# Kernel optimization log

Hardware: AMD Instinct MI355X
Metric: run time of the kernel (lower is better)

## Reference

```python
import jax, jax.numpy as jnp
import numpy as np

# Irreps layout: 128x0e + 64x1o + 32x2e  (mul, 2l+1)
MULS = [128, 64, 32]
DEGS = [1, 3, 5]
D = sum(m * d for m, d in zip(MULS, DEGS))  # 480
N = 200_000
G = 1000


def _split(x):
    """[N, D] -> list of [N, mul, deg] irrep blocks."""
    out, o = [], 0
    for m, d in zip(MULS, DEGS):
        out.append(x[:, o:o + m * d].reshape(-1, m, d))
        o += m * d
    return out


def _merge(blocks):
    return jnp.concatenate([b.reshape(b.shape[0], -1) for b in blocks], axis=-1)


def _equiv_linear(xb, Ws):
    """e3nn-style per-irrep channel-mixing linear with 1/sqrt(fan_in) norm."""
    return [jnp.einsum('nmd,mo->nod', x, W) / np.float32(np.sqrt(m))
            for x, W, m in zip(xb, Ws, MULS)]


def setup_inputs() -> dict:
    key = jax.random.key(0)
    ks = jax.random.split(key, 16)
    inp = {"f": jax.random.normal(ks[0], (N, D), jnp.float32)}
    i = 1
    for name in ["Wq", "Wk", "Wv", "Wd"]:
        for j, m in enumerate(MULS):
            inp[f"{name}{j}"] = jax.random.normal(ks[i], (m, m), jnp.float32)
            i += 1
    inp["batch"] = jnp.sort(jax.random.randint(ks[15], (N,), 0, G))
    inp["n_graphs"] = G
    return inp


def reference(f, Wq0, Wq1, Wq2, Wk0, Wk1, Wk2, Wv0, Wv1, Wv2,
              Wd0, Wd1, Wd2, batch, n_graphs):
    fb = _split(f)
    qb = _equiv_linear(fb, [Wq0, Wq1, Wq2])
    kb = _equiv_linear(fb, [Wk0, Wk1, Wk2])
    vb = _equiv_linear(fb, [Wv0, Wv1, Wv2])

    # FullyConnectedTensorProduct(q, k, '0e'): only paths with matching l
    # contribute; each path is a weighted channel-pair dot over m components.
    logits = jnp.zeros(f.shape[0], f.dtype)
    for q, k, W, m, d in zip(qb, kb, [Wd0, Wd1, Wd2], MULS, DEGS):
        logits = logits + jnp.einsum('nid,njd,ij->n', q, k, W) / np.float32(np.sqrt(m * m * d))
    logits = logits / np.float32(np.sqrt(len(MULS)))  # path-count normalization
    logits = logits * np.float32(1.0 / np.sqrt(D))    # self.scale buffer

    w = jnp.exp(logits)                                       # [N]
    norm = jax.ops.segment_sum(w, batch, num_segments=n_graphs)
    norm = jnp.clip(norm, 1e-8)
    v = _merge(vb)                                            # [N, D]
    num = jax.ops.segment_sum(v * w[:, None], batch, num_segments=n_graphs)
    return num / norm[:, None]                                # [G, D]
```

## Files before the change

kernel.cpp:

```cpp
#include <hip/hip_runtime.h>
#include <math.h>

#define D_TOT 480

typedef short bf16x8 __attribute__((ext_vector_type(8)));
typedef float f32x4 __attribute__((ext_vector_type(4)));

#define MFMA16(a, b, c) __builtin_amdgcn_mfma_f32_16x16x32_bf16((a), (b), (c), 0, 0, 0)

static __device__ __forceinline__ unsigned short f2bf(float x) {
  unsigned u = __float_as_uint(x);
  u += 0x7FFFu + ((u >> 16) & 1u);
  return (unsigned short)(u >> 16);
}

template <int M, int DEG, int BASE>
static __device__ void precompute_impl(
    const float* __restrict__ Wq, const float* __restrict__ Wk,
    const float* __restrict__ Wd, const float* __restrict__ Wv,
    unsigned short* __restrict__ Bp, int kt, float* lds) {
  float* sWkT = lds;
  float* sT   = lds + M * (M + 1);

  constexpr int TPR = 256 / M;
  constexpr int RPT = 32 / TPR;
  constexpr int nct = M / 8;
  constexpr int ktn = M / 32;

  int t = threadIdx.x;
  float scale = 1.0f / ((float)M * (float)M * sqrtf(1440.0f * (float)DEG));
  float sm = rsqrtf((float)M);

  for (int i = t; i < M * M; i += 256) {
    int r = i / M, c = i - r * M;
    sWkT[c * (M + 1) + r] = Wk[i];
  }

  {
    int c = t % M, r0 = t / M;
    float acc[RPT];
#pragma unroll
    for (int rr = 0; rr < RPT; ++rr) acc[rr] = 0.f;
#pragma unroll 4
    for (int a = 0; a < M; ++a) {
      float wd = Wd[a * M + c];
#pragma unroll
      for (int rr = 0; rr < RPT; ++rr)
        acc[rr] += Wq[(kt * 32 + r0 + rr * TPR) * M + a] * wd;
    }
    __syncthreads();
#pragma unroll
    for (int rr = 0; rr < RPT; ++rr) sT[(r0 + rr * TPR) * M + c] = acc[rr];
  }
  __syncthreads();

  {
    int j = t % M, r0 = t / M;
    float acc[RPT];
#pragma unroll
    for (int rr = 0; rr < RPT; ++rr) acc[rr] = 0.f;
#pragma unroll 4
    for (int c = 0; c < M; ++c) {
      float wk = sWkT[c * (M + 1) + j];
#pragma unroll
      for (int rr = 0; rr < RPT; ++rr)
        acc[rr] += sT[(r0 + rr * TPR) * M + c] * wk;
    }
    __syncthreads();
#pragma unroll
    for (int rr = 0; rr < RPT; ++rr) sT[(r0 + rr * TPR) * M + j] = acc[rr] * scale;
  }
  __syncthreads();

  for (int idx = t; idx < nct * 512; idx += 256) {
    int ct = idx >> 9, rem = idx & 511, l = rem >> 3, j = rem & 7;
    int kl = (l >> 4) * 8 + j;
    int c = ct * 16 + (l & 15);
    float val = (c < M) ? sT[kl * M + c] : Wv[(kt * 32 + kl) * M + (c - M)] * sm;
    Bp[BASE + (ct * ktn + kt) * 512 + rem] = f2bf(val);
  }
}

__global__ __launch_bounds__(256) void precompute_all(
    const float* __restrict__ Wq0, const float* __restrict__ Wq1, const float* __restrict__ Wq2,
    const float* __restrict__ Wk0, const float* __restrict__ Wk1, const float* __restrict__ Wk2,
    const float* __restrict__ Wd0, const float* __restrict__ Wd1, const float* __restrict__ Wd2,
    const float* __restrict__ Wv0, const float* __restrict__ Wv1, const float* __restrict__ Wv2,
    unsigned short* __restrict__ Bp) {
  extern __shared__ float lds[];
  int b = blockIdx.x;
  if (b < 4)      precompute_impl<128, 1, 0>(Wq0, Wk0, Wd0, Wv0, Bp, b, lds);
  else if (b < 6) precompute_impl<64, 3, 32768>(Wq1, Wk1, Wd1, Wv1, Bp, b - 4, lds);
  else            precompute_impl<32, 5, 40960>(Wq2, Wk2, Wd2, Wv2, Bp, 0, lds);
}

__global__ __launch_bounds__(256, 2) void fused_stat_kernel(
    const float* __restrict__ f, const unsigned short* __restrict__ Bpack,
    const int* __restrict__ batch,
    float* __restrict__ outnum, float* __restrict__ norm,
    int N, int tpb, int ntiles) {
  __shared__ float lds_logit[3][16];
  int t = threadIdx.x, w = t >> 6, lane = t & 63;
  int q = lane >> 4, lm = lane & 15;

  if (t < 48) ((float*)lds_logit)[t] = 0.f;
  __syncthreads();

  int t0 = blockIdx.x * tpb;
  int t1 = min(t0 + tpb, ntiles);
  if (t0 >= t1) return;

  const bf16x8* B0f = (const bf16x8*)Bpack;
  const bf16x8* B1f = (const bf16x8*)(Bpack + 32768);
  const bf16x8* B2f = (const bf16x8*)(Bpack + 40960);

  bf16x8 Bu0[2][4], Bv0[2][4], Bu1[2], Bv1[2], Bu2, Bv2;
#pragma unroll
  for (int ctl = 0; ctl < 2; ++ctl)
#pragma unroll
    for (int k = 0; k < 4; ++k) {
      Bu0[ctl][k] = B0f[((2 * w + ctl) * 4 + k) * 64 + lane];
      Bv0[ctl][k] = B0f[((2 * w + ctl + 8) * 4 + k) * 64 + lane];
    }
#pragma unroll
  for (int k = 0; k < 2; ++k) {
    Bu1[k] = B1f[(w * 2 + k) * 64 + lane];
    Bv1[k] = B1f[((w + 4) * 2 + k) * 64 + lane];
  }
  bool has2 = (w >= 2);
  int ct2 = has2 ? (w - 2) : 0;
  Bu2 = B2f[ct2 * 64 + lane];
  Bv2 = B2f[(ct2 + 2) * 64 + lane];

  float racc0[2] = {0.f, 0.f};
  float racc1[3] = {0.f, 0.f, 0.f};
  float racc2[5] = {0.f, 0.f, 0.f, 0.f, 0.f};
  float naccw = 0.f;
  int cur_g = -1;

  auto wavered = [&](float s) -> float {
    s += __shfl_xor(s, 16);
    s += __shfl_xor(s, 32);
    return s;
  };
  auto flushf = [&](int g) {
    float* og = outnum + (size_t)g * 480;
#pragma unroll
    for (int ctl = 0; ctl < 2; ++ctl) {
      float s = wavered(racc0[ctl]);
      if (lane < 16) atomicAdd(og + (2 * w + ctl) * 16 + lane, s);
      racc0[ctl] = 0.f;
    }
#pragma unroll
    for (int d = 0; d < 3; ++d) {
      float s = wavered(racc1[d]);
      if (lane < 16) atomicAdd(og + 128 + 3 * (w * 16 + lane) + d, s);
      racc1[d] = 0.f;
    }
    if (has2) {
#pragma unroll
      for (int d = 0; d < 5; ++d) {
        float s = wavered(racc2[d]);
        if (lane < 16) atomicAdd(og + 320 + 5 * (ct2 * 16 + lane) + d, s);
        racc2[d] = 0.f;
      }
    }
    if (w == 0) {
      float s = wavered(naccw);
      if (lane == 0) atomicAdd(norm + g, s);
      naccw = 0.f;
    }
  };

  for (int ti = t0; ti < t1; ++ti) {
    int p = ti % 3;
    int nt = ti * 16;
    int valid = min(16, N - nt);

    long rr = nt + (lm < valid ? lm : valid - 1);
    const float4* fr4 = reinterpret_cast<const float4*>(f + rr * 480);
    bf16x8 a0[4], a1[3][2], a2[5];
#pragma unroll
    for (int ks = 0; ks < 4; ++ks) {
      float4 A = fr4[ks * 8 + 2 * q];
      float4 B = fr4[ks * 8 + 2 * q + 1];
      bf16x8 v;
      v[0] = (short)f2bf(A.x); v[1] = (short)f2bf(A.y);
      v[2] = (short)f2bf(A.z); v[3] = (short)f2bf(A.w);
      v[4] = (short)f2bf(B.x); v[5] = (short)f2bf(B.y);
      v[6] = (short)f2bf(B.z); v[7] = (short)f2bf(B.w);
      a0[ks] = v;
    }
#pragma unroll
    for (int h = 0; h < 2; ++h) {
      unsigned short bb[24];
#pragma unroll
      for (int i = 0; i < 6; ++i) {
        float4 x4 = fr4[32 + 24 * h + 6 * q + i];
        bb[i * 4 + 0] = f2bf(x4.x); bb[i * 4 + 1] = f2bf(x4.y);
        bb[i * 4 + 2] = f2bf(x4.z); bb[i * 4 + 3] = f2bf(x4.w);
      }
#pragma unroll
      for (int d = 0; d < 3; ++d) {
        bf16x8 v;
#pragma unroll
        for (int j = 0; j < 8; ++j) v[j] = (short)bb[3 * j + d];
        a1[d][h] = v;
      }
    }
    {
      unsigned short bb[40];
#pragma unroll
      for (int i = 0; i < 10; ++i) {
        float4 x4 = fr4[80 + 10 * q + i];
        bb[i * 4 + 0] = f2bf(x4.x); bb[i * 4 + 1] = f2bf(x4.y);
        bb[i * 4 + 2] = f2bf(x4.z); bb[i * 4 + 3] = f2bf(x4.w);
      }
#pragma unroll
      for (int d = 0; d < 5; ++d) {
        bf16x8 v;
#pragma unroll
        for (int j = 0; j < 8; ++j) v[j] = (short)bb[5 * j + d];
        a2[d] = v;
      }
    }

    auto xg = [&](int r, int c) -> float {
      int nn = nt + q * 4 + r;
      if (nn >= N) nn = N - 1;
      return f[(size_t)nn * 480 + c];
    };

    float pl[4] = {0.f, 0.f, 0.f, 0.f};
#pragma unroll
    for (int ctl = 0; ctl < 2; ++ctl) {
      f32x4 u = {0.f, 0.f, 0.f, 0.f};
      u = MFMA16(a0[0], Bu0[ctl][0], u);
      u = MFMA16(a0[1], Bu0[ctl][1], u);
      u = MFMA16(a0[2], Bu0[ctl][2], u);
      u = MFMA16(a0[3], Bu0[ctl][3], u);
      int c = (2 * w + ctl) * 16 + lm;
#pragma unroll
      for (int r = 0; r < 4; ++r) pl[r] += u[r] * xg(r, c);
    }
#pragma unroll
    for (int d = 0; d < 3; ++d) {
      f32x4 u = {0.f, 0.f, 0.f, 0.f};
      u = MFMA16(a1[d][0], Bu1[0], u);
      u = MFMA16(a1[d][1], Bu1[1], u);
      int c = 128 + 3 * (w * 16 + lm) + d;
#pragma unroll
      for (int r = 0; r < 4; ++r) pl[r] += u[r] * xg(r, c);
    }
    if (has2) {
#pragma unroll
      for (int d = 0; d < 5; ++d) {
        f32x4 u = {0.f, 0.f, 0.f, 0.f};
        u = MFMA16(a2[d], Bu2, u);
        int c = 320 + 5 * (ct2 * 16 + lm) + d;
#pragma unroll
        for (int r = 0; r < 4; ++r) pl[r] += u[r] * xg(r, c);
      }
    }
#pragma unroll
    for (int off = 1; off < 16; off <<= 1) {
#pragma unroll
      for (int r = 0; r < 4; ++r) pl[r] += __shfl_xor(pl[r], off);
    }
    if (lm == 0) {
#pragma unroll
      for (int r = 0; r < 4; ++r) atomicAdd(&lds_logit[p][q * 4 + r], pl[r]);
    }
    __syncthreads();

    float wgt[4];
#pragma unroll
    for (int r = 0; r < 4; ++r) {
      int node = q * 4 + r;
      wgt[r] = (node < valid) ? __expf(lds_logit[p][node]) : 0.f;
    }
    if (t < 16) lds_logit[(ti + 2) % 3][t] = 0.f;

    {
      int nn = nt + (lm < valid ? lm : valid - 1);
      if (nn >= N) nn = N - 1;
      int gl = batch[nn];
      int gp = __shfl(gl, (lane == 0) ? 0 : lane - 1);
      unsigned long long bm = __ballot(lm > 0 && lm < valid && gl != gp);
      unsigned segm = (unsigned)bm & 0xFFFEu;

      int a = 0;
      while (a < valid) {
        unsigned hi = segm & ~((1u << (a + 1)) - 1u);
        int b = hi ? (int)__builtin_ctz(hi) : valid;
        int gs = __shfl(gl, a);
        if (gs != cur_g) {
          if (cur_g >= 0) flushf(cur_g);
          cur_g = gs;
        }
        int nq = q * 4;
        float m0 = (nq + 0 >= a && nq + 0 < b) ? wgt[0] : 0.f;
        float m1 = (nq + 1 >= a && nq + 1 < b) ? wgt[1] : 0.f;
        float m2 = (nq + 2 >= a && nq + 2 < b) ? wgt[2] : 0.f;
        float m3 = (nq + 3 >= a && nq + 3 < b) ? wgt[3] : 0.f;
        if (w == 0 && lm == 0) naccw += m0 + m1 + m2 + m3;
#pragma unroll
        for (int ctl = 0; ctl < 2; ++ctl) {
          f32x4 v = {0.f, 0.f, 0.f, 0.f};
          v = MFMA16(a0[0], Bv0[ctl][0], v);
          v = MFMA16(a0[1], Bv0[ctl][1], v);
          v = MFMA16(a0[2], Bv0[ctl][2], v);
          v = MFMA16(a0[3], Bv0[ctl][3], v);
          racc0[ctl] += m0 * v[0] + m1 * v[1] + m2 * v[2] + m3 * v[3];
        }
#pragma unroll
        for (int d = 0; d < 3; ++d) {
          f32x4 v = {0.f, 0.f, 0.f, 0.f};
          v = MFMA16(a1[d][0], Bv1[0], v);
          v = MFMA16(a1[d][1], Bv1[1], v);
          racc1[d] += m0 * v[0] + m1 * v[1] + m2 * v[2] + m3 * v[3];
        }
        if (has2) {
#pragma unroll
          for (int d = 0; d < 5; ++d) {
            f32x4 v = {0.f, 0.f, 0.f, 0.f};
            v = MFMA16(a2[d], Bv2, v);
            racc2[d] += m0 * v[0] + m1 * v[1] + m2 * v[2] + m3 * v[3];
          }
        }
        a = b;
      }
    }
  }
  if (cur_g >= 0) flushf(cur_g);
}

__global__ __launch_bounds__(256) void finalize_kernel(
    float* __restrict__ out, const float* __restrict__ norm, int total) {
  int idx = blockIdx.x * blockDim.x + threadIdx.x;
  if (idx < total) {
    int g = idx / 480;
    out[idx] = out[idx] / fmaxf(norm[g], 1e-8f);
  }
}

extern "C" void kernel_launch(void* const* d_in, const int* in_sizes, int n_in,
                              void* d_out, int out_size, void* d_ws, size_t ws_size,
                              hipStream_t stream) {
  const float* f   = (const float*)d_in[0];
  const int* batch = (const int*)d_in[13];

  int N = in_sizes[0] / D_TOT;
  int G = out_size / D_TOT;

  unsigned short* Bpack = (unsigned short*)d_ws;
  float* norm = (float*)((char*)d_ws + 86016);
  float* out  = (float*)d_out;

  hipMemsetAsync(d_out, 0, (size_t)out_size * sizeof(float), stream);
  hipMemsetAsync(norm, 0, (size_t)G * sizeof(float), stream);

  int lds128 = (128 * 129 + 32 * 128) * 4;
  hipFuncSetAttribute((const void*)precompute_all,
                      hipFuncAttributeMaxDynamicSharedMemorySize, lds128);
  precompute_all<<<7, 256, lds128, stream>>>(
      (const float*)d_in[1], (const float*)d_in[2], (const float*)d_in[3],
      (const float*)d_in[4], (const float*)d_in[5], (const float*)d_in[6],
      (const float*)d_in[10], (const float*)d_in[11], (const float*)d_in[12],
      (const float*)d_in[7], (const float*)d_in[8], (const float*)d_in[9],
      Bpack);

  int ntiles = (N + 15) / 16;
  int nblocks = 1024;
  if (nblocks > ntiles) nblocks = ntiles;
  int tpb = (ntiles + nblocks - 1) / nblocks;

  fused_stat_kernel<<<nblocks, 256, 0, stream>>>(
      f, Bpack, batch, out, norm, N, tpb, ntiles);

  finalize_kernel<<<(G * D_TOT + 255) / 256, 256, 0, stream>>>(out, norm, G * D_TOT);
}
```

Baseline: 309.7 us.

## Double-buffer input tiles in LDS via async global_load_lds with XOR swizzle

Each 16-row input tile is now staged into a double-buffered, XOR-swizzled LDS buffer with asynchronous global-to-LDS loads, and the next tile is prefetched while the current one is computed. All A-operand packing and the per-element gathers for the logits now read from LDS rather than global memory. The grid is halved to 512 blocks, which gives each block more tiles to pipeline. This uses about 60 KB of LDS per block, which can limit occupancy. It also relies on correct barrier placement, since the initial barrier was removed and there is no explicit wait on the async loads.

```diff
diff --git a/kernel.cpp b/kernel.cpp
--- a/kernel.cpp
+++ b/kernel.cpp
@@ -35,7 +35,6 @@
     int r = i / M, c = i - r * M;
     sWkT[c * (M + 1) + r] = Wk[i];
   }
-
   {
     int c = t % M, r0 = t / M;
     float acc[RPT];
@@ -53,7 +52,6 @@
     for (int rr = 0; rr < RPT; ++rr) sT[(r0 + rr * TPR) * M + c] = acc[rr];
   }
   __syncthreads();
-
   {
     int j = t % M, r0 = t / M;
     float acc[RPT];
@@ -71,7 +69,6 @@
     for (int rr = 0; rr < RPT; ++rr) sT[(r0 + rr * TPR) * M + j] = acc[rr] * scale;
   }
   __syncthreads();
-
   for (int idx = t; idx < nct * 512; idx += 256) {
     int ct = idx >> 9, rem = idx & 511, l = rem >> 3, j = rem & 7;
     int kl = (l >> 4) * 8 + j;
@@ -99,12 +96,12 @@
     const int* __restrict__ batch,
     float* __restrict__ outnum, float* __restrict__ norm,
     int N, int tpb, int ntiles) {
+  __shared__ __align__(16) char xsmem[2 * 30720];
   __shared__ float lds_logit[3][16];
   int t = threadIdx.x, w = t >> 6, lane = t & 63;
   int q = lane >> 4, lm = lane & 15;
 
   if (t < 48) ((float*)lds_logit)[t] = 0.f;
-  __syncthreads();
 
   int t0 = blockIdx.x * tpb;
   int t1 = min(t0 + tpb, ntiles);
@@ -131,6 +128,26 @@
   int ct2 = has2 ? (w - 2) : 0;
   Bu2 = B2f[ct2 * 64 + lane];
   Bv2 = B2f[(ct2 + 2) * 64 + lane];
+
+  auto stage = [&](int buf, int ti2) {
+    int nt2 = ti2 * 16;
+    int vmax = min(16, N - nt2) - 1;
+    char* dstbase = xsmem + buf * 30720;
+#pragma unroll
+    for (int k = 0; k < 8; ++k) {
+      int i = w + 4 * k;
+      if (i >= 30) break;
+      int D = i * 64 + lane;
+      int r = D / 120;
+      int g = (D - r * 120) ^ (r & 7);
+      int rc = r < vmax ? r : vmax;
+      const float* src = f + (size_t)(nt2 + rc) * 480 + g * 4;
+      __builtin_amdgcn_global_load_lds(
+          (const __attribute__((address_space(1))) void*)src,
+          (__attribute__((address_space(3))) void*)(dstbase + i * 1024),
+          16, 0, 0);
+    }
+  };
 
   float racc0[2] = {0.f, 0.f};
   float racc1[3] = {0.f, 0.f, 0.f};
@@ -172,18 +189,31 @@
     }
   };
 
-  for (int ti = t0; ti < t1; ++ti) {
+  stage(0, t0);
+
+  int cur = 0;
+  for (int ti = t0; ti < t1; ++ti, cur ^= 1) {
     int p = ti % 3;
     int nt = ti * 16;
     int valid = min(16, N - nt);
 
-    long rr = nt + (lm < valid ? lm : valid - 1);
-    const float4* fr4 = reinterpret_cast<const float4*>(f + rr * 480);
+    __syncthreads();
+    if (ti + 1 < t1) stage(cur ^ 1, ti + 1);
+
+    const char* xcur = xsmem + cur * 30720;
+    auto ld4 = [&](int r, int gr) -> float4 {
+      return *reinterpret_cast<const float4*>(xcur + r * 1920 + ((gr ^ (r & 7)) << 4));
+    };
+    auto ldf = [&](int r, int c) -> float {
+      return *reinterpret_cast<const float*>(
+          xcur + r * 1920 + ((((c >> 2)) ^ (r & 7)) << 4) + ((c & 3) << 2));
+    };
+
     bf16x8 a0[4], a1[3][2], a2[5];
 #pragma unroll
     for (int ks = 0; ks < 4; ++ks) {
-      float4 A = fr4[ks * 8 + 2 * q];
-      float4 B = fr4[ks * 8 + 2 * q + 1];
+      float4 A = ld4(lm, ks * 8 + 2 * q);
+      float4 B = ld4(lm, ks * 8 + 2 * q + 1);
       bf16x8 v;
       v[0] = (short)f2bf(A.x); v[1] = (short)f2bf(A.y);
       v[2] = (short)f2bf(A.z); v[3] = (short)f2bf(A.w);
@@ -192,44 +222,23 @@
       a0[ks] = v;
     }
 #pragma unroll
-    for (int h = 0; h < 2; ++h) {
-      unsigned short bb[24];
-#pragma unroll
-      for (int i = 0; i < 6; ++i) {
-        float4 x4 = fr4[32 + 24 * h + 6 * q + i];
-        bb[i * 4 + 0] = f2bf(x4.x); bb[i * 4 + 1] = f2bf(x4.y);
-        bb[i * 4 + 2] = f2bf(x4.z); bb[i * 4 + 3] = f2bf(x4.w);
-      }
-#pragma unroll
-      for (int d = 0; d < 3; ++d) {
+    for (int d = 0; d < 3; ++d)
+#pragma unroll
+      for (int h = 0; h < 2; ++h) {
         bf16x8 v;
 #pragma unroll
-        for (int j = 0; j < 8; ++j) v[j] = (short)bb[3 * j + d];
+        for (int j = 0; j < 8; ++j)
+          v[j] = (short)f2bf(ldf(lm, 128 + 3 * (h * 32 + q * 8 + j) + d));
         a1[d][h] = v;
       }
-    }
-    {
-      unsigned short bb[40];
-#pragma unroll
-      for (int i = 0; i < 10; ++i) {
-        float4 x4 = fr4[80 + 10 * q + i];
-        bb[i * 4 + 0] = f2bf(x4.x); bb[i * 4 + 1] = f2bf(x4.y);
-        bb[i * 4 + 2] = f2bf(x4.z); bb[i * 4 + 3] = f2bf(x4.w);
-      }
-#pragma unroll
-      for (int d = 0; d < 5; ++d) {
-        bf16x8 v;
-#pragma unroll
-        for (int j = 0; j < 8; ++j) v[j] = (short)bb[5 * j + d];
-        a2[d] = v;
-      }
-    }
-
-    auto xg = [&](int r, int c) -> float {
-      int nn = nt + q * 4 + r;
-      if (nn >= N) nn = N - 1;
-      return f[(size_t)nn * 480 + c];
-    };
+#pragma unroll
+    for (int d = 0; d < 5; ++d) {
+      bf16x8 v;
+#pragma unroll
+      for (int j = 0; j < 8; ++j)
+        v[j] = (short)f2bf(ldf(lm, 320 + 5 * (q * 8 + j) + d));
+      a2[d] = v;
+    }
 
     float pl[4] = {0.f, 0.f, 0.f, 0.f};
 #pragma unroll
@@ -241,7 +250,7 @@
       u = MFMA16(a0[3], Bu0[ctl][3], u);
       int c = (2 * w + ctl) * 16 + lm;
 #pragma unroll
-      for (int r = 0; r < 4; ++r) pl[r] += u[r] * xg(r, c);
+      for (int r = 0; r < 4; ++r) pl[r] += u[r] * ldf(q * 4 + r, c);
     }
 #pragma unroll
     for (int d = 0; d < 3; ++d) {
@@ -250,7 +259,7 @@
       u = MFMA16(a1[d][1], Bu1[1], u);
       int c = 128 + 3 * (w * 16 + lm) + d;
 #pragma unroll
-      for (int r = 0; r < 4; ++r) pl[r] += u[r] * xg(r, c);
+      for (int r = 0; r < 4; ++r) pl[r] += u[r] * ldf(q * 4 + r, c);
     }
     if (has2) {
 #pragma unroll
@@ -259,7 +268,7 @@
         u = MFMA16(a2[d], Bu2, u);
         int c = 320 + 5 * (ct2 * 16 + lm) + d;
 #pragma unroll
-        for (int r = 0; r < 4; ++r) pl[r] += u[r] * xg(r, c);
+        for (int r = 0; r < 4; ++r) pl[r] += u[r] * ldf(q * 4 + r, c);
       }
     }
 #pragma unroll
@@ -371,7 +380,7 @@
       Bpack);
 
   int ntiles = (N + 15) / 16;
-  int nblocks = 1024;
+  int nblocks = 512;
   if (nblocks > ntiles) nblocks = ntiles;
   int tpb = (ntiles + nblocks - 1) / nblocks;
 
```

Measured after the change: 582.6 us. +88.1%, slower.
